# Kernel optimization log

Hardware: AMD Instinct MI355X
Metric: run time of the kernel (lower is better)

The kernel has to match this reference:

```python
import jax, jax.numpy as jnp
import numpy as np

HEADS = 4
WS = 4
EPS = 1e-5

def _pw(x, w, b):
    # 1x1 conv: w is (out_c, in_c)
    return jnp.einsum('oc,bchw->bohw', w, x) + b[None, :, None, None]

def _dw(x, w, b, stride):
    # depthwise 5x5 conv, padding 2; w is (C,1,5,5) OIHW with groups=C
    c = x.shape[1]
    y = jax.lax.conv_general_dilated(x, w, (stride, stride), [(2, 2), (2, 2)],
                                     feature_group_count=c,
                                     dimension_numbers=('NCHW', 'OIHW', 'NCHW'))
    return y + b[None, :, None, None]

def _bn(x, g, bt, m, v):
    # inference-mode batchnorm
    return (x - m[None, :, None, None]) * (g / jnp.sqrt(v + EPS))[None, :, None, None] + bt[None, :, None, None]

def _fasa(x, q_w, q_b, kv_w, kv_b, local_w, local_b, mixer_w, mixer_b,
          p0_w, p0_b, bn0_g, bn0_b, bn0_m, bn0_v, lin0_w, lin0_b,
          p1_w, p1_b, bn1_g, bn1_b, bn1_m, bn1_v):
    b, c, h, w = x.shape
    H, W = h // WS, w // WS
    dh = c // HEADS
    q_local = _pw(x, q_w, q_b)
    # refined_downsample pool: dwconv(s2)+bn+1x1, dwconv(s2)+bn
    p = _dw(x, p0_w, p0_b, 2)
    p = _bn(p, bn0_g, bn0_b, bn0_m, bn0_v)
    p = _pw(p, lin0_w, lin0_b)
    p = _dw(p, p1_w, p1_b, 2)
    p = _bn(p, bn1_g, bn1_b, bn1_m, bn1_v)
    kv = _pw(p, kv_w, kv_b)                               # (b, 2c, H, W)
    q = q_local.reshape(b, HEADS, dh, h * w).transpose(0, 1, 3, 2)   # (b,h,hw,dh)
    kv = kv.reshape(b, 2, HEADS, dh, H * W).transpose(1, 0, 2, 4, 3) # (2,b,h,HW,dh)
    k, v = kv[0], kv[1]
    scale = dh ** -0.5
    attn = jax.nn.softmax(scale * jnp.einsum('bhqd,bhkd->bhqk', q, k), axis=-1)
    gf = jnp.einsum('bhqk,bhkd->bhqd', attn, v)           # (b,h,hw,dh)
    gf = gf.transpose(0, 1, 3, 2).reshape(b, c, h, w)
    lf = _dw(q_local, local_w, local_b, 1)
    lf = lf * jax.nn.sigmoid(lf)        # local_feat * local_weight
    lf = lf * jax.nn.sigmoid(gf)        # local_feat * local2global
    return _pw(lf * gf, mixer_w, mixer_b)

def setup_inputs() -> dict:
    key = jax.random.key(0)
    ks = jax.random.split(key, 24)
    B, C, Hh, Ww, K = 4, 128, 128, 128, 5
    s = 0.05
    d = {
        'x': jax.random.normal(ks[0], (B, C, Hh, Ww), jnp.float32),
        'q_w': jax.random.normal(ks[1], (C, C), jnp.float32) * s,
        'q_b': jnp.zeros((C,), jnp.float32),
        'kv_w': jax.random.normal(ks[2], (2 * C, C), jnp.float32) * s,
        'kv_b': jnp.zeros((2 * C,), jnp.float32),
        'local_w': jax.random.normal(ks[3], (C, 1, K, K), jnp.float32) * s,
        'local_b': jnp.zeros((C,), jnp.float32),
        'mixer_w': jax.random.normal(ks[4], (C, C), jnp.float32) * s,
        'mixer_b': jnp.zeros((C,), jnp.float32),
        'p0_w': jax.random.normal(ks[5], (C, 1, K, K), jnp.float32) * s,
        'p0_b': jnp.zeros((C,), jnp.float32),
        'bn0_g': jnp.ones((C,), jnp.float32),
        'bn0_b': jnp.zeros((C,), jnp.float32),
        'bn0_m': jax.random.normal(ks[6], (C,), jnp.float32) * 0.1,
        'bn0_v': jax.random.uniform(ks[7], (C,), jnp.float32) + 0.5,
        'lin0_w': jax.random.normal(ks[8], (C, C), jnp.float32) * s,
        'lin0_b': jnp.zeros((C,), jnp.float32),
        'p1_w': jax.random.normal(ks[9], (C, 1, K, K), jnp.float32) * s,
        'p1_b': jnp.zeros((C,), jnp.float32),
        'bn1_g': jnp.ones((C,), jnp.float32),
        'bn1_b': jnp.zeros((C,), jnp.float32),
        'bn1_m': jax.random.normal(ks[10], (C,), jnp.float32) * 0.1,
        'bn1_v': jax.random.uniform(ks[11], (C,), jnp.float32) + 0.5,
    }
    return d

def reference(x, q_w, q_b, kv_w, kv_b, local_w, local_b, mixer_w, mixer_b,
              p0_w, p0_b, bn0_g, bn0_b, bn0_m, bn0_v, lin0_w, lin0_b,
              p1_w, p1_b, bn1_g, bn1_b, bn1_m, bn1_v):
    return _fasa(x, q_w, q_b, kv_w, kv_b, local_w, local_b, mixer_w, mixer_b,
                 p0_w, p0_b, bn0_g, bn0_b, bn0_m, bn0_v, lin0_w, lin0_b,
                 p1_w, p1_b, bn1_g, bn1_b, bn1_m, bn1_v)
```

## Files before the change

kernel.cpp:

```cpp
#include <hip/hip_runtime.h>
#include <hip/hip_bf16.h>
#include <math.h>


#define NB   4
#define NC   128
#define NH   128
#define NW   128
#define NHW  16384
#define NKV  1024

typedef float    f32x4  __attribute__((ext_vector_type(4)));
typedef float    f32x16 __attribute__((ext_vector_type(16)));
typedef short    bf16x8 __attribute__((ext_vector_type(8)));
typedef unsigned u32x4v __attribute__((ext_vector_type(4)));

__device__ __forceinline__ unsigned short f2bf(float f) {
  unsigned u = __float_as_uint(f);
  u += 0x7FFF + ((u >> 16) & 1);
  return (unsigned short)(u >> 16);
}

__device__ __forceinline__ unsigned cvtpk(float lo, float hi) {
  unsigned r;
  asm("v_cvt_pk_bf16_f32 %0, %1, %2" : "=v"(r) : "v"(lo), "v"(hi));
  return r;
}

__global__ __launch_bounds__(256) void pw_gemm_mfma(
    const float* __restrict__ Wmat,
    const float* __restrict__ bias,
    const float* __restrict__ X,
    float* __restrict__ Y,
    int npos)
{
  __shared__ short Wlds[128 * 136];

  const int t  = threadIdx.x;
  const int w    = t >> 6;
  const int lane = t & 63;
  const int nl   = lane & 31;
  const int hi   = lane >> 5;
  const int b  = blockIdx.z;
  const int m0 = blockIdx.y * 128;
  const int n0 = blockIdx.x * 128;
  const int Mtot = gridDim.y * 128;

  for (int i = t; i < 128 * 32; i += 256) {
    int row = i >> 5, c4 = (i & 31) * 4;
    float4 wv = *(const float4*)&Wmat[(size_t)(m0 + row) * 128 + c4];
    uint2 pk; pk.x = cvtpk(wv.x, wv.y); pk.y = cvtpk(wv.z, wv.w);
    *(uint2*)&Wlds[row * 136 + c4] = pk;
  }
  __syncthreads();

  const float* Xb = X + (size_t)b * 128 * npos + n0 + w * 32 + nl;

  f32x16 acc[4];
  #pragma unroll
  for (int mg = 0; mg < 4; mg++)
    #pragma unroll
    for (int r = 0; r < 16; r++) acc[mg][r] = 0.f;

  #pragma unroll
  for (int s = 0; s < 8; s++) {
    const float* xp = Xb + (size_t)(s * 16 + hi * 8) * npos;
    float xv[8];
    #pragma unroll
    for (int e = 0; e < 8; e++) xv[e] = xp[(size_t)e * npos];
    u32x4v bu;
    #pragma unroll
    for (int j = 0; j < 4; j++) bu[j] = cvtpk(xv[2 * j], xv[2 * j + 1]);
    bf16x8 bfrag = __builtin_bit_cast(bf16x8, bu);

    #pragma unroll
    for (int mg = 0; mg < 4; mg++) {
      bf16x8 afrag = *(const bf16x8*)&Wlds[(mg * 32 + nl) * 136 + s * 16 + hi * 8];
      acc[mg] = __builtin_amdgcn_mfma_f32_32x32x16_bf16(afrag, bfrag, acc[mg], 0, 0, 0);
    }
  }

  float* Yb = Y + ((size_t)b * Mtot + m0) * npos + n0 + w * 32 + nl;
  #pragma unroll
  for (int mg = 0; mg < 4; mg++)
    #pragma unroll
    for (int r = 0; r < 16; r++) {
      int drow = mg * 32 + (r & 3) + 8 * (r >> 2) + 4 * hi;
      Yb[(size_t)drow * npos] = acc[mg][r] + bias[m0 + drow];
    }
}

template<int INH, int INW, int OUTW, int ORPB, int WLSP>
__global__ __launch_bounds__(256) void dw5x5s2_tile(
    const float* __restrict__ in,
    const float* __restrict__ wt, const float* __restrict__ bias,
    const float* __restrict__ g, const float* __restrict__ bt,
    const float* __restrict__ mean, const float* __restrict__ var,
    float* __restrict__ out)
{
  constexpr int IR = 2 * ORPB + 3;
  constexpr int XG = OUTW / 4;
  __shared__ float Ls[IR * WLSP];

  const int t  = threadIdx.x;
  const int c  = blockIdx.y, b = blockIdx.z;
  const int y0 = blockIdx.x * ORPB;
  const float* plane = in + ((size_t)b * NC + c) * INH * INW;

  for (int i = t; i < IR * WLSP / 4; i += 256)
    *(float4*)&Ls[i * 4] = (float4){0.f, 0.f, 0.f, 0.f};
  __syncthreads();

  for (int i = t; i < IR * (INW / 4); i += 256) {
    int r = i / (INW / 4), s4 = (i % (INW / 4)) * 4;
    int gy = 2 * y0 - 2 + r;
    if (gy >= 0 && gy < INH)
      *(float4*)&Ls[r * WLSP + 4 + s4] = *(const float4*)&plane[(size_t)gy * INW + s4];
  }

  float wreg[25];
  #pragma unroll
  for (int i = 0; i < 25; i++) wreg[i] = wt[c * 25 + i];
  const float sc = g[c] * rsqrtf(var[c] + 1e-5f);
  const float off = (bias[c] - mean[c]) * sc + bt[c];
  __syncthreads();

  const int row = t / XG;
  const int x0  = (t % XG) * 4;
  const int r0  = 2 * row;

  float a[4] = {0.f, 0.f, 0.f, 0.f};
  #pragma unroll
  for (int i = 0; i < 5; i++) {
    const float* lr = &Ls[(r0 + i) * WLSP + 2 * x0];
    float4 L0 = *(const float4*)&lr[0];
    float4 L1 = *(const float4*)&lr[4];
    float4 L2 = *(const float4*)&lr[8];
    float4 L3 = *(const float4*)&lr[12];
    float rr[16] = {L0.x,L0.y,L0.z,L0.w, L1.x,L1.y,L1.z,L1.w,
                    L2.x,L2.y,L2.z,L2.w, L3.x,L3.y,L3.z,L3.w};
    #pragma unroll
    for (int j = 0; j < 5; j++) {
      float wv = wreg[i * 5 + j];
      #pragma unroll
      for (int o = 0; o < 4; o++)
        a[o] += wv * rr[2 * o + j + 2];
    }
  }

  float4 ov;
  ov.x = a[0] * sc + off; ov.y = a[1] * sc + off;
  ov.z = a[2] * sc + off; ov.w = a[3] * sc + off;
  const int OH = INH / 2;
  *(float4*)&out[((size_t)b * NC + c) * OH * OUTW + (size_t)(y0 + row) * OUTW + x0] = ov;
}

__global__ __launch_bounds__(256) void kv_prep(
    const float* __restrict__ kvb,
    short* __restrict__ kT, short* __restrict__ vT)
{
  const int t = threadIdx.x;
  const int h = blockIdx.y, b = blockIdx.z;
  const int kpos = blockIdx.x * 256 + t;
  const int bh = b * 4 + h;

  bf16x8 kr[4];
  #pragma unroll
  for (int d = 0; d < 32; d++) {
    float kvv = kvb[((size_t)b * 256 + h * 32 + d) * NKV + kpos];
    float vvv = kvb[((size_t)b * 256 + 128 + h * 32 + d) * NKV + kpos];
    kr[d >> 3][d & 7] = (short)f2bf(kvv);
    vT[(size_t)bh * 32768 + d * NKV + kpos] = (short)f2bf(vvv);
  }
  short* dstk = kT + (size_t)bh * 32768 + (size_t)kpos * 32;
  #pragma unroll
  for (int i = 0; i < 4; i++)
    *(bf16x8*)(dstk + i * 8) = kr[i];
}

__global__ __launch_bounds__(256) void attn_mfma64(
    const float* __restrict__ q_local,
    const short* __restrict__ kT,
    const short* __restrict__ vT,
    float* __restrict__ gf)
{
  const int t    = threadIdx.x;
  const int w    = t >> 6;
  const int lane = t & 63;
  const int c    = lane & 31;
  const int hi   = lane >> 5;
  const int b    = blockIdx.z, h = blockIdx.y;
  const int q0   = blockIdx.x * 256 + w * 64;
  const int bh   = b * 4 + h;

  const float QSCALE = 0.17677669529663689f * 1.4426950408889634f;

  bf16x8 qA1, qA2, qB1, qB2;
  {
    const float* qb = q_local + ((size_t)(b * NC + h * 32 + hi * 8)) * NHW + q0 + c;
    float fva[16], fvb[16];
    #pragma unroll
    for (int e = 0; e < 8; e++) {
      fva[e]     = qb[(size_t)e * NHW] * QSCALE;
      fva[8 + e] = qb[(size_t)(16 + e) * NHW] * QSCALE;
      fvb[e]     = qb[(size_t)e * NHW + 32] * QSCALE;
      fvb[8 + e] = qb[(size_t)(16 + e) * NHW + 32] * QSCALE;
    }
    u32x4v u1, u2, u3, u4;
    #pragma unroll
    for (int j = 0; j < 4; j++) {
      u1[j] = cvtpk(fva[2 * j], fva[2 * j + 1]);
      u2[j] = cvtpk(fva[8 + 2 * j], fva[9 + 2 * j]);
      u3[j] = cvtpk(fvb[2 * j], fvb[2 * j + 1]);
      u4[j] = cvtpk(fvb[8 + 2 * j], fvb[9 + 2 * j]);
    }
    qA1 = __builtin_bit_cast(bf16x8, u1); qA2 = __builtin_bit_cast(bf16x8, u2);
    qB1 = __builtin_bit_cast(bf16x8, u3); qB2 = __builtin_bit_cast(bf16x8, u4);
  }

  const short* kbh = kT + (size_t)bh * 32768;
  const short* vbh = vT + (size_t)bh * 32768;

  f32x16 oA, oB;
  #pragma unroll
  for (int r = 0; r < 16; r++) { oA[r] = 0.f; oB[r] = 0.f; }
  const f32x16 zf = oA;
  float lsumA = 0.f, lsumB = 0.f;

  bf16x8 ka  = *(const bf16x8*)(kbh + (size_t)c * 32 + hi * 8);
  bf16x8 kb2 = *(const bf16x8*)(kbh + (size_t)c * 32 + 16 + hi * 8);
  bf16x8 va  = *(const bf16x8*)(vbh + (size_t)c * NKV + hi * 8);
  bf16x8 vb2 = *(const bf16x8*)(vbh + (size_t)c * NKV + 16 + hi * 8);

  for (int kt = 0; kt < 32; kt++) {
    const int k0n = (kt < 31) ? (kt + 1) * 32 : 0;
    bf16x8 nka  = *(const bf16x8*)(kbh + (size_t)(k0n + c) * 32 + hi * 8);
    bf16x8 nkb  = *(const bf16x8*)(kbh + (size_t)(k0n + c) * 32 + 16 + hi * 8);
    bf16x8 nva  = *(const bf16x8*)(vbh + (size_t)c * NKV + k0n + hi * 8);
    bf16x8 nvb  = *(const bf16x8*)(vbh + (size_t)c * NKV + k0n + 16 + hi * 8);

    {
      f32x16 s = __builtin_amdgcn_mfma_f32_32x32x16_bf16(ka,  qA1, zf, 0, 0, 0);
      s        = __builtin_amdgcn_mfma_f32_32x32x16_bf16(kb2, qA2, s,  0, 0, 0);
      float p[16];
      #pragma unroll
      for (int r = 0; r < 16; r++) p[r] = __builtin_amdgcn_exp2f(s[r]);
      float s0 = (p[0] + p[1]) + (p[2] + p[3]);
      float s1 = (p[4] + p[5]) + (p[6] + p[7]);
      float s2 = (p[8] + p[9]) + (p[10] + p[11]);
      float s3 = (p[12] + p[13]) + (p[14] + p[15]);
      lsumA += (s0 + s1) + (s2 + s3);

      unsigned a0 = cvtpk(p[0],  p[1]);
      unsigned a1 = cvtpk(p[2],  p[3]);
      unsigned a2 = cvtpk(p[4],  p[5]);
      unsigned a3 = cvtpk(p[6],  p[7]);
      unsigned a4 = cvtpk(p[8],  p[9]);
      unsigned a5 = cvtpk(p[10], p[11]);
      unsigned a6 = cvtpk(p[12], p[13]);
      unsigned a7 = cvtpk(p[14], p[15]);
      asm("v_permlane32_swap_b32 %0, %1" : "+v"(a0), "+v"(a2));
      asm("v_permlane32_swap_b32 %0, %1" : "+v"(a1), "+v"(a3));
      asm("v_permlane32_swap_b32 %0, %1" : "+v"(a4), "+v"(a6));
      asm("v_permlane32_swap_b32 %0, %1" : "+v"(a5), "+v"(a7));
      u32x4v b1u = {a0, a1, a2, a3};
      u32x4v b2u = {a4, a5, a6, a7};
      bf16x8 pb1 = __builtin_bit_cast(bf16x8, b1u);
      bf16x8 pb2 = __builtin_bit_cast(bf16x8, b2u);
      oA = __builtin_amdgcn_mfma_f32_32x32x16_bf16(va,  pb1, oA, 0, 0, 0);
      oA = __builtin_amdgcn_mfma_f32_32x32x16_bf16(vb2, pb2, oA, 0, 0, 0);
    }

    {
      f32x16 s = __builtin_amdgcn_mfma_f32_32x32x16_bf16(ka,  qB1, zf, 0, 0, 0);
      s        = __builtin_amdgcn_mfma_f32_32x32x16_bf16(kb2, qB2, s,  0, 0, 0);
      float p[16];
      #pragma unroll
      for (int r = 0; r < 16; r++) p[r] = __builtin_amdgcn_exp2f(s[r]);
      float s0 = (p[0] + p[1]) + (p[2] + p[3]);
      float s1 = (p[4] + p[5]) + (p[6] + p[7]);
      float s2 = (p[8] + p[9]) + (p[10] + p[11]);
      float s3 = (p[12] + p[13]) + (p[14] + p[15]);
      lsumB += (s0 + s1) + (s2 + s3);

      unsigned a0 = cvtpk(p[0],  p[1]);
      unsigned a1 = cvtpk(p[2],  p[3]);
      unsigned a2 = cvtpk(p[4],  p[5]);
      unsigned a3 = cvtpk(p[6],  p[7]);
      unsigned a4 = cvtpk(p[8],  p[9]);
      unsigned a5 = cvtpk(p[10], p[11]);
      unsigned a6 = cvtpk(p[12], p[13]);
      unsigned a7 = cvtpk(p[14], p[15]);
      asm("v_permlane32_swap_b32 %0, %1" : "+v"(a0), "+v"(a2));
      asm("v_permlane32_swap_b32 %0, %1" : "+v"(a1), "+v"(a3));
      asm("v_permlane32_swap_b32 %0, %1" : "+v"(a4), "+v"(a6));
      asm("v_permlane32_swap_b32 %0, %1" : "+v"(a5), "+v"(a7));
      u32x4v b1u = {a0, a1, a2, a3};
      u32x4v b2u = {a4, a5, a6, a7};
      bf16x8 pb1 = __builtin_bit_cast(bf16x8, b1u);
      bf16x8 pb2 = __builtin_bit_cast(bf16x8, b2u);
      oB = __builtin_amdgcn_mfma_f32_32x32x16_bf16(va,  pb1, oB, 0, 0, 0);
      oB = __builtin_amdgcn_mfma_f32_32x32x16_bf16(vb2, pb2, oB, 0, 0, 0);
    }

    ka = nka; kb2 = nkb; va = nva; vb2 = nvb;
  }

  lsumA += __shfl_xor(lsumA, 32);
  lsumB += __shfl_xor(lsumB, 32);
  float invA = 1.f / lsumA;
  float invB = 1.f / lsumB;

  float* gfb = gf + ((size_t)(b * NC + h * 32)) * NHW + q0 + c;
  #pragma unroll
  for (int r = 0; r < 16; r++) {
    int d = (r & 3) + 8 * (r >> 2) + 4 * hi;
    gfb[(size_t)d * NHW]      = oA[r] * invA;
    gfb[(size_t)d * NHW + 32] = oB[r] * invB;
  }
}

__global__ __launch_bounds__(256) void lf_fuse_tile(
    const float* __restrict__ qloc, const float* __restrict__ gf,
    const float* __restrict__ wt, const float* __restrict__ bias,
    float* __restrict__ tout)
{
  __shared__ float Ls[12 * 140];

  const int t  = threadIdx.x;
  const int c  = blockIdx.y, b = blockIdx.z;
  const int y0 = blockIdx.x * 8;
  const float* plane = qloc + ((size_t)b * NC + c) * NHW;

  for (int i = t; i < 12 * 140 / 4; i += 256)
    *(float4*)&Ls[i * 4] = (float4){0.f, 0.f, 0.f, 0.f};
  __syncthreads();

  for (int i = t; i < 12 * 32; i += 256) {
    int r = i >> 5, s4 = (i & 31) * 4;
    int gy = y0 - 2 + r;
    if (gy >= 0 && gy < NH)
      *(float4*)&Ls[r * 140 + 4 + s4] = *(const float4*)&plane[(size_t)gy * NW + s4];
  }

  float wreg[25];
  #pragma unroll
  for (int i = 0; i < 25; i++) wreg[i] = wt[c * 25 + i];
  const float bs = bias[c];
  __syncthreads();

  const int row = t >> 5;
  const int x0  = (t & 31) * 4;

  float a[4] = {bs, bs, bs, bs};
  #pragma unroll
  for (int i = 0; i < 5; i++) {
    const float* lr = &Ls[(row + i) * 140 + x0];
    float4 L0 = *(const float4*)&lr[0];
    float4 L1 = *(const float4*)&lr[4];
    float4 L2 = *(const float4*)&lr[8];
    float rr[12] = {L0.x,L0.y,L0.z,L0.w, L1.x,L1.y,L1.z,L1.w,
                    L2.x,L2.y,L2.z,L2.w};
    #pragma unroll
    for (int j = 0; j < 5; j++) {
      float wv = wreg[i * 5 + j];
      #pragma unroll
      for (int o = 0; o < 4; o++)
        a[o] += wv * rr[o + j + 2];
    }
  }

  size_t base = ((size_t)b * NC + c) * NHW + (size_t)(y0 + row) * NW + x0;
  float4 gv4 = *(const float4*)&gf[base];
  float gvv[4] = {gv4.x, gv4.y, gv4.z, gv4.w};
  float4 ov;
  float* op = (float*)&ov;
  #pragma unroll
  for (int k = 0; k < 4; k++) {
    float sl = a[k] / (1.f + __expf(-a[k]));
    float sg = 1.f / (1.f + __expf(-gvv[k]));
    op[k] = sl * sg * gvv[k];
  }
  *(float4*)&tout[base] = ov;
}

extern "C" void kernel_launch(void* const* d_in, const int* in_sizes, int n_in,
                              void* d_out, int out_size, void* d_ws, size_t ws_size,
                              hipStream_t stream) {
  const float* x       = (const float*)d_in[0];
  const float* q_w     = (const float*)d_in[1];
  const float* q_b     = (const float*)d_in[2];
  const float* kv_w    = (const float*)d_in[3];
  const float* kv_b    = (const float*)d_in[4];
  const float* local_w = (const float*)d_in[5];
  const float* local_b = (const float*)d_in[6];
  const float* mixer_w = (const float*)d_in[7];
  const float* mixer_b = (const float*)d_in[8];
  const float* p0_w    = (const float*)d_in[9];
  const float* p0_b    = (const float*)d_in[10];
  const float* bn0_g   = (const float*)d_in[11];
  const float* bn0_b   = (const float*)d_in[12];
  const float* bn0_m   = (const float*)d_in[13];
  const float* bn0_v   = (const float*)d_in[14];
  const float* lin0_w  = (const float*)d_in[15];
  const float* lin0_b  = (const float*)d_in[16];
  const float* p1_w    = (const float*)d_in[17];
  const float* p1_b    = (const float*)d_in[18];
  const float* bn1_g   = (const float*)d_in[19];
  const float* bn1_b   = (const float*)d_in[20];
  const float* bn1_m   = (const float*)d_in[21];
  const float* bn1_v   = (const float*)d_in[22];

  float* ws = (float*)d_ws;
  float* q_local = ws;
  float* gf      = ws + 8388608;
  float* tbuf    = ws + 16777216;
  float* p0      = ws + 25165824;
  float* lin0b   = ws + 27262976;
  float* p1      = ws + 29360128;
  float* kvb     = ws + 29884416;
  short* kT      = (short*)(ws + 30932992);
  short* vT      = kT + 524288;

  pw_gemm_mfma<<<dim3(NHW / 128, 1, NB), 256, 0, stream>>>(q_w, q_b, x, q_local, NHW);
  dw5x5s2_tile<128, 128, 64, 16, 140><<<dim3(4, NC, NB), 256, 0, stream>>>(
      x, p0_w, p0_b, bn0_g, bn0_b, bn0_m, bn0_v, p0);
  pw_gemm_mfma<<<dim3(4096 / 128, 1, NB), 256, 0, stream>>>(lin0_w, lin0_b, p0, lin0b, 4096);
  dw5x5s2_tile<64, 64, 32, 32, 76><<<dim3(1, NC, NB), 256, 0, stream>>>(
      lin0b, p1_w, p1_b, bn1_g, bn1_b, bn1_m, bn1_v, p1);
  pw_gemm_mfma<<<dim3(NKV / 128, 2, NB), 256, 0, stream>>>(kv_w, kv_b, p1, kvb, NKV);
  kv_prep<<<dim3(4, 4, NB), 256, 0, stream>>>(kvb, kT, vT);
  attn_mfma64<<<dim3(NHW / 256, 4, NB), 256, 0, stream>>>(q_local, kT, vT, gf);
  lf_fuse_tile<<<dim3(16, NC, NB), 256, 0, stream>>>(q_local, gf, local_w, local_b, tbuf);
  pw_gemm_mfma<<<dim3(NHW / 128, 1, NB), 256, 0, stream>>>(mixer_w, mixer_b, tbuf, (float*)d_out, NHW);
}
```

Baseline: 168.4 us.

## Store q_local and mixer input as bf16, split attention keys across two waves

The q projection now writes its output as bf16, and the local-feature fuse kernel writes its output as bf16. The attention, depthwise and mixer GEMM kernels read these bf16 buffers, which halves the memory traffic of two large intermediate tensors. The attention kernel now runs 512 threads per block: each group of four waves processes half of the keys, and the partial outputs and softmax sums are combined through LDS before normalising. This adds extra rounding of q_local before the local depthwise conv and extra LDS synchronisation in exchange for more parallelism per query tile.

Result: faster. 153.4 us (-8.9%).

```diff
diff --git a/kernel.cpp b/kernel.cpp
--- a/kernel.cpp
+++ b/kernel.cpp
@@ -21,18 +21,23 @@
   return (unsigned short)(u >> 16);
 }
 
+__device__ __forceinline__ float bf2f(unsigned short u) {
+  return __uint_as_float((unsigned)u << 16);
+}
+
 __device__ __forceinline__ unsigned cvtpk(float lo, float hi) {
   unsigned r;
   asm("v_cvt_pk_bf16_f32 %0, %1, %2" : "=v"(r) : "v"(lo), "v"(hi));
   return r;
 }
 
+template<bool IN_BF16, bool OUT_BF16>
 __global__ __launch_bounds__(256) void pw_gemm_mfma(
     const float* __restrict__ Wmat,
     const float* __restrict__ bias,
-    const float* __restrict__ X,
-    float* __restrict__ Y,
-    int npos)
+    const void* __restrict__ Xv,
+    void* __restrict__ Yv,
+    int npos, int Mtot)
 {
   __shared__ short Wlds[128 * 136];
 
@@ -44,7 +49,6 @@
   const int b  = blockIdx.z;
   const int m0 = blockIdx.y * 128;
   const int n0 = blockIdx.x * 128;
-  const int Mtot = gridDim.y * 128;
 
   for (int i = t; i < 128 * 32; i += 256) {
     int row = i >> 5, c4 = (i & 31) * 4;
@@ -54,8 +58,6 @@
   }
   __syncthreads();
 
-  const float* Xb = X + (size_t)b * 128 * npos + n0 + w * 32 + nl;
-
   f32x16 acc[4];
   #pragma unroll
   for (int mg = 0; mg < 4; mg++)
@@ -64,14 +66,24 @@
 
   #pragma unroll
   for (int s = 0; s < 8; s++) {
-    const float* xp = Xb + (size_t)(s * 16 + hi * 8) * npos;
-    float xv[8];
-    #pragma unroll
-    for (int e = 0; e < 8; e++) xv[e] = xp[(size_t)e * npos];
-    u32x4v bu;
-    #pragma unroll
-    for (int j = 0; j < 4; j++) bu[j] = cvtpk(xv[2 * j], xv[2 * j + 1]);
-    bf16x8 bfrag = __builtin_bit_cast(bf16x8, bu);
+    bf16x8 bfrag;
+    if constexpr (IN_BF16) {
+      const unsigned short* Xb = (const unsigned short*)Xv
+          + (size_t)b * 128 * npos + n0 + w * 32 + nl;
+      const unsigned short* xp = Xb + (size_t)(s * 16 + hi * 8) * npos;
+      #pragma unroll
+      for (int e = 0; e < 8; e++) bfrag[e] = (short)xp[(size_t)e * npos];
+    } else {
+      const float* Xb = (const float*)Xv + (size_t)b * 128 * npos + n0 + w * 32 + nl;
+      const float* xp = Xb + (size_t)(s * 16 + hi * 8) * npos;
+      float xv[8];
+      #pragma unroll
+      for (int e = 0; e < 8; e++) xv[e] = xp[(size_t)e * npos];
+      u32x4v bu;
+      #pragma unroll
+      for (int j = 0; j < 4; j++) bu[j] = cvtpk(xv[2 * j], xv[2 * j + 1]);
+      bfrag = __builtin_bit_cast(bf16x8, bu);
+    }
 
     #pragma unroll
     for (int mg = 0; mg < 4; mg++) {
@@ -80,13 +92,20 @@
     }
   }
 
-  float* Yb = Y + ((size_t)b * Mtot + m0) * npos + n0 + w * 32 + nl;
   #pragma unroll
   for (int mg = 0; mg < 4; mg++)
     #pragma unroll
     for (int r = 0; r < 16; r++) {
       int drow = mg * 32 + (r & 3) + 8 * (r >> 2) + 4 * hi;
-      Yb[(size_t)drow * npos] = acc[mg][r] + bias[m0 + drow];
+      float val = acc[mg][r] + bias[m0 + drow];
+      if constexpr (OUT_BF16) {
+        unsigned short* Yb = (unsigned short*)Yv
+            + ((size_t)b * Mtot + m0) * npos + n0 + w * 32 + nl;
+        Yb[(size_t)drow * npos] = f2bf(val);
+      } else {
+        float* Yb = (float*)Yv + ((size_t)b * Mtot + m0) * npos + n0 + w * 32 + nl;
+        Yb[(size_t)drow * npos] = val;
+      }
     }
 }
 
@@ -178,33 +197,38 @@
     *(bf16x8*)(dstk + i * 8) = kr[i];
 }
 
-__global__ __launch_bounds__(256) void attn_mfma64(
-    const float* __restrict__ q_local,
+__global__ __launch_bounds__(512) void attn_mfma64(
+    const unsigned short* __restrict__ q16,
     const short* __restrict__ kT,
     const short* __restrict__ vT,
     float* __restrict__ gf)
 {
+  __shared__ float Cmb[4][64][34];
+
   const int t    = threadIdx.x;
   const int w    = t >> 6;
   const int lane = t & 63;
   const int c    = lane & 31;
   const int hi   = lane >> 5;
+  const int qg   = w & 3;
+  const int half = w >> 2;
   const int b    = blockIdx.z, h = blockIdx.y;
-  const int q0   = blockIdx.x * 256 + w * 64;
+  const int q0   = blockIdx.x * 256 + qg * 64;
   const int bh   = b * 4 + h;
+  const int base = half * 16;
 
   const float QSCALE = 0.17677669529663689f * 1.4426950408889634f;
 
   bf16x8 qA1, qA2, qB1, qB2;
   {
-    const float* qb = q_local + ((size_t)(b * NC + h * 32 + hi * 8)) * NHW + q0 + c;
+    const unsigned short* qb = q16 + ((size_t)(b * NC + h * 32 + hi * 8)) * NHW + q0 + c;
     float fva[16], fvb[16];
     #pragma unroll
     for (int e = 0; e < 8; e++) {
-      fva[e]     = qb[(size_t)e * NHW] * QSCALE;
-      fva[8 + e] = qb[(size_t)(16 + e) * NHW] * QSCALE;
-      fvb[e]     = qb[(size_t)e * NHW + 32] * QSCALE;
-      fvb[8 + e] = qb[(size_t)(16 + e) * NHW + 32] * QSCALE;
+      fva[e]     = bf2f(qb[(size_t)e * NHW]) * QSCALE;
+      fva[8 + e] = bf2f(qb[(size_t)(16 + e) * NHW]) * QSCALE;
+      fvb[e]     = bf2f(qb[(size_t)e * NHW + 32]) * QSCALE;
+      fvb[8 + e] = bf2f(qb[(size_t)(16 + e) * NHW + 32]) * QSCALE;
     }
     u32x4v u1, u2, u3, u4;
     #pragma unroll
@@ -227,13 +251,14 @@
   const f32x16 zf = oA;
   float lsumA = 0.f, lsumB = 0.f;
 
-  bf16x8 ka  = *(const bf16x8*)(kbh + (size_t)c * 32 + hi * 8);
-  bf16x8 kb2 = *(const bf16x8*)(kbh + (size_t)c * 32 + 16 + hi * 8);
-  bf16x8 va  = *(const bf16x8*)(vbh + (size_t)c * NKV + hi * 8);
-  bf16x8 vb2 = *(const bf16x8*)(vbh + (size_t)c * NKV + 16 + hi * 8);
-
-  for (int kt = 0; kt < 32; kt++) {
-    const int k0n = (kt < 31) ? (kt + 1) * 32 : 0;
+  const int kbase = base * 32;
+  bf16x8 ka  = *(const bf16x8*)(kbh + (size_t)(kbase + c) * 32 + hi * 8);
+  bf16x8 kb2 = *(const bf16x8*)(kbh + (size_t)(kbase + c) * 32 + 16 + hi * 8);
+  bf16x8 va  = *(const bf16x8*)(vbh + (size_t)c * NKV + kbase + hi * 8);
+  bf16x8 vb2 = *(const bf16x8*)(vbh + (size_t)c * NKV + kbase + 16 + hi * 8);
+
+  for (int kt = 0; kt < 16; kt++) {
+    const int k0n = (kt < 15) ? (kbase + (kt + 1) * 32) : 0;
     bf16x8 nka  = *(const bf16x8*)(kbh + (size_t)(k0n + c) * 32 + hi * 8);
     bf16x8 nkb  = *(const bf16x8*)(kbh + (size_t)(k0n + c) * 32 + 16 + hi * 8);
     bf16x8 nva  = *(const bf16x8*)(vbh + (size_t)c * NKV + k0n + hi * 8);
@@ -306,41 +331,59 @@
     ka = nka; kb2 = nkb; va = nva; vb2 = nvb;
   }
 
-  lsumA += __shfl_xor(lsumA, 32);
-  lsumB += __shfl_xor(lsumB, 32);
-  float invA = 1.f / lsumA;
-  float invB = 1.f / lsumB;
-
-  float* gfb = gf + ((size_t)(b * NC + h * 32)) * NHW + q0 + c;
-  #pragma unroll
-  for (int r = 0; r < 16; r++) {
-    int d = (r & 3) + 8 * (r >> 2) + 4 * hi;
-    gfb[(size_t)d * NHW]      = oA[r] * invA;
-    gfb[(size_t)d * NHW + 32] = oB[r] * invB;
+  if (half) {
+    float* dst = &Cmb[qg][lane][0];
+    #pragma unroll
+    for (int r = 0; r < 16; r++) { dst[r] = oA[r]; dst[16 + r] = oB[r]; }
+    dst[32] = lsumA; dst[33] = lsumB;
+  }
+  __syncthreads();
+  if (!half) {
+    const float* src = &Cmb[qg][lane][0];
+    #pragma unroll
+    for (int r = 0; r < 16; r++) { oA[r] += src[r]; oB[r] += src[16 + r]; }
+    lsumA += src[32]; lsumB += src[33];
+
+    lsumA += __shfl_xor(lsumA, 32);
+    lsumB += __shfl_xor(lsumB, 32);
+    float invA = 1.f / lsumA;
+    float invB = 1.f / lsumB;
+
+    float* gfb = gf + ((size_t)(b * NC + h * 32)) * NHW + q0 + c;
+    #pragma unroll
+    for (int r = 0; r < 16; r++) {
+      int d = (r & 3) + 8 * (r >> 2) + 4 * hi;
+      gfb[(size_t)d * NHW]      = oA[r] * invA;
+      gfb[(size_t)d * NHW + 32] = oB[r] * invB;
+    }
   }
 }
 
 __global__ __launch_bounds__(256) void lf_fuse_tile(
-    const float* __restrict__ qloc, const float* __restrict__ gf,
+    const unsigned short* __restrict__ q16, const float* __restrict__ gf,
     const float* __restrict__ wt, const float* __restrict__ bias,
-    float* __restrict__ tout)
+    unsigned short* __restrict__ t16)
 {
   __shared__ float Ls[12 * 140];
 
   const int t  = threadIdx.x;
   const int c  = blockIdx.y, b = blockIdx.z;
   const int y0 = blockIdx.x * 8;
-  const float* plane = qloc + ((size_t)b * NC + c) * NHW;
+  const unsigned short* plane = q16 + ((size_t)b * NC + c) * NHW;
 
   for (int i = t; i < 12 * 140 / 4; i += 256)
     *(float4*)&Ls[i * 4] = (float4){0.f, 0.f, 0.f, 0.f};
   __syncthreads();
 
-  for (int i = t; i < 12 * 32; i += 256) {
-    int r = i >> 5, s4 = (i & 31) * 4;
+  for (int i = t; i < 12 * 16; i += 256) {
+    int r = i >> 4, s8 = (i & 15) * 8;
     int gy = y0 - 2 + r;
-    if (gy >= 0 && gy < NH)
-      *(float4*)&Ls[r * 140 + 4 + s4] = *(const float4*)&plane[(size_t)gy * NW + s4];
+    if (gy >= 0 && gy < NH) {
+      bf16x8 v = *(const bf16x8*)&plane[(size_t)gy * NW + s8];
+      float* dp = &Ls[r * 140 + 4 + s8];
+      #pragma unroll
+      for (int j = 0; j < 8; j++) dp[j] = bf2f((unsigned short)v[j]);
+    }
   }
 
   float wreg[25];
@@ -373,15 +416,17 @@
   size_t base = ((size_t)b * NC + c) * NHW + (size_t)(y0 + row) * NW + x0;
   float4 gv4 = *(const float4*)&gf[base];
   float gvv[4] = {gv4.x, gv4.y, gv4.z, gv4.w};
-  float4 ov;
-  float* op = (float*)&ov;
+  float op[4];
   #pragma unroll
   for (int k = 0; k < 4; k++) {
     float sl = a[k] / (1.f + __expf(-a[k]));
     float sg = 1.f / (1.f + __expf(-gvv[k]));
     op[k] = sl * sg * gvv[k];
   }
-  *(float4*)&tout[base] = ov;
+  uint2 ov;
+  ov.x = cvtpk(op[0], op[1]);
+  ov.y = cvtpk(op[2], op[3]);
+  *(uint2*)&t16[base] = ov;
 }
 
 extern "C" void kernel_launch(void* const* d_in, const int* in_sizes, int n_in,
@@ -412,25 +457,29 @@
   const float* bn1_v   = (const float*)d_in[22];
 
   float* ws = (float*)d_ws;
-  float* q_local = ws;
-  float* gf      = ws + 8388608;
-  float* tbuf    = ws + 16777216;
-  float* p0      = ws + 25165824;
-  float* lin0b   = ws + 27262976;
-  float* p1      = ws + 29360128;
-  float* kvb     = ws + 29884416;
-  short* kT      = (short*)(ws + 30932992);
-  short* vT      = kT + 524288;
-
-  pw_gemm_mfma<<<dim3(NHW / 128, 1, NB), 256, 0, stream>>>(q_w, q_b, x, q_local, NHW);
+  unsigned short* q16 = (unsigned short*)ws;
+  float* gf   = ws + 4194304;
+  unsigned short* t16 = (unsigned short*)(ws + 12582912);
+  float* p0   = ws + 16777216;
+  float* lin0b= ws + 18874368;
+  float* p1   = ws + 20971520;
+  float* kvb  = ws + 21495808;
+  short* kT   = (short*)(ws + 22544384);
+  short* vT   = kT + 524288;
+
+  pw_gemm_mfma<false, true><<<dim3(NHW / 128, 1, NB), 256, 0, stream>>>(
+      q_w, q_b, x, q16, NHW, 128);
   dw5x5s2_tile<128, 128, 64, 16, 140><<<dim3(4, NC, NB), 256, 0, stream>>>(
       x, p0_w, p0_b, bn0_g, bn0_b, bn0_m, bn0_v, p0);
-  pw_gemm_mfma<<<dim3(4096 / 128, 1, NB), 256, 0, stream>>>(lin0_w, lin0_b, p0, lin0b, 4096);
+  pw_gemm_mfma<false, false><<<dim3(4096 / 128, 1, NB), 256, 0, stream>>>(
+      lin0_w, lin0_b, p0, lin0b, 4096, 128);
   dw5x5s2_tile<64, 64, 32, 32, 76><<<dim3(1, NC, NB), 256, 0, stream>>>(
       lin0b, p1_w, p1_b, bn1_g, bn1_b, bn1_m, bn1_v, p1);
-  pw_gemm_mfma<<<dim3(NKV / 128, 2, NB), 256, 0, stream>>>(kv_w, kv_b, p1, kvb, NKV);
+  pw_gemm_mfma<false, false><<<dim3(NKV / 128, 2, NB), 256, 0, stream>>>(
+      kv_w, kv_b, p1, kvb, NKV, 256);
   kv_prep<<<dim3(4, 4, NB), 256, 0, stream>>>(kvb, kT, vT);
-  attn_mfma64<<<dim3(NHW / 256, 4, NB), 256, 0, stream>>>(q_local, kT, vT, gf);
-  lf_fuse_tile<<<dim3(16, NC, NB), 256, 0, stream>>>(q_local, gf, local_w, local_b, tbuf);
-  pw_gemm_mfma<<<dim3(NHW / 128, 1, NB), 256, 0, stream>>>(mixer_w, mixer_b, tbuf, (float*)d_out, NHW);
-}
+  attn_mfma64<<<dim3(NHW / 256, 4, NB), 512, 0, stream>>>(q16, kT, vT, gf);
+  lf_fuse_tile<<<dim3(16, NC, NB), 256, 0, stream>>>(q16, gf, local_w, local_b, t16);
+  pw_gemm_mfma<true, false><<<dim3(NHW / 128, 1, NB), 256, 0, stream>>>(
+      mixer_w, mixer_b, t16, (float*)d_out, NHW, 128);
+}
```
